# Kernel tuning notes

Measured on AMD Instinct MI355X. Metric: run time of the kernel, lower is better.

## Reference

```python
import math
import jax, jax.numpy as jnp
import numpy as np

B, T, S, H, L, NH = 2, 512, 2048, 768, 32, 12
INTERMED = 4 * H


def _make_pe(max_len, hidden):
    position = np.arange(max_len)[:, None].astype(np.float32)
    div_term = np.exp(np.arange(0, hidden, 2).astype(np.float32) * (-math.log(10000.0) / hidden))
    pe = np.zeros((max_len, hidden), dtype=np.float32)
    pe[:, 0::2] = np.sin(position * div_term)
    pe[:, 1::2] = np.cos(position * div_term)
    return jnp.asarray(pe)


def setup_inputs() -> dict:
    key = jax.random.key(0)
    ks = jax.random.split(key, 10)
    token_reps = jax.random.normal(ks[0], (B, T, H), dtype=jnp.float32)
    starts = jax.random.randint(ks[1], (B, S), 0, T - L)
    lens = jax.random.randint(ks[2], (B, S), 1, L + 1)
    span_ids = jnp.stack([starts, starts + lens], axis=-1)  # (B,S,2)
    span_masks = jax.random.uniform(ks[3], (B, S)) > 0.2
    pe = _make_pe(T, H)
    dummy_query = jax.random.normal(ks[4], (H,), dtype=jnp.float32) * 0.02
    in_proj_w = jax.random.normal(ks[5], (3 * H, H), dtype=jnp.float32) * 0.02
    in_proj_b = jnp.zeros((3 * H,), jnp.float32)
    out_proj_w = jax.random.normal(ks[6], (H, H), dtype=jnp.float32) * 0.02
    out_proj_b = jnp.zeros((H,), jnp.float32)
    norm_g = jnp.ones((H,), jnp.float32)
    norm_b = jnp.zeros((H,), jnp.float32)
    ffn_w1 = jax.random.normal(ks[7], (INTERMED, H), dtype=jnp.float32) * (math.sqrt(2.0 / H))
    ffn_b1 = jnp.zeros((INTERMED,), jnp.float32)
    ffn_w2 = jax.random.normal(ks[8], (H, INTERMED), dtype=jnp.float32) * (math.sqrt(2.0 / INTERMED))
    ffn_b2 = jnp.zeros((H,), jnp.float32)
    return dict(token_reps=token_reps, span_ids=span_ids, span_masks=span_masks,
                pooling=0, pe=pe, dummy_query=dummy_query,
                in_proj_w=in_proj_w, in_proj_b=in_proj_b,
                out_proj_w=out_proj_w, out_proj_b=out_proj_b,
                norm_g=norm_g, norm_b=norm_b,
                ffn_w1=ffn_w1, ffn_b1=ffn_b1, ffn_w2=ffn_w2, ffn_b2=ffn_b2)


def _layernorm(x, g, b, eps=1e-5):
    mu = jnp.mean(x, axis=-1, keepdims=True)
    var = jnp.mean(jnp.square(x - mu), axis=-1, keepdims=True)
    return (x - mu) * jax.lax.rsqrt(var + eps) * g + b


def reference(token_reps, span_ids, span_masks, pooling, pe, dummy_query,
              in_proj_w, in_proj_b, out_proj_w, out_proj_b,
              norm_g, norm_b, ffn_w1, ffn_b1, ffn_w2, ffn_b2):
    b, t, h = token_reps.shape
    s = span_ids.shape[1]
    hd = h // NH
    # positional encoding over the sequence (dropout=0 / eval mode)
    x = token_reps + pe[:t]
    # ragged -> padded gather of span tokens
    starts = span_ids[..., 0]
    lens = (span_ids[..., 1] - starts) * span_masks.astype(span_ids.dtype)  # (B,S)
    ar = jnp.arange(L)
    pos = starts[..., None] + ar                     # (B,S,L)
    valid = ar[None, None, :] < lens[..., None]      # (B,S,L) True = real token
    idx = jnp.clip(pos, 0, t - 1)
    gathered = jax.vmap(lambda xb, ib: xb[ib])(x, idx)   # (B,S,L,H)
    gathered = gathered * valid[..., None]
    # guard fully-masked rows (masked-out / zero-len spans): keep one key valid,
    # output is zeroed at the end anyway (matches torch span_reps[~mask]=0)
    any_v = jnp.any(valid, axis=-1)
    valid = valid.at[..., 0].set(valid[..., 0] | ~any_v)
    # single-query multi-head attention (torch nn.MultiheadAttention math)
    Wq, Wk, Wv = jnp.split(in_proj_w, 3, axis=0)
    bq, bk, bv = jnp.split(in_proj_b, 3, axis=0)
    q = (dummy_query @ Wq.T + bq).reshape(NH, hd)                  # (NH,hd)
    k = (gathered @ Wk.T + bk).reshape(b, s, L, NH, hd)
    v = (gathered @ Wv.T + bv).reshape(b, s, L, NH, hd)
    scores = jnp.einsum('nd,bslnd->bsnl', q, k) / math.sqrt(hd)    # (B,S,NH,L)
    scores = jnp.where(valid[:, :, None, :], scores, -jnp.inf)
    attn = jax.nn.softmax(scores, axis=-1)
    ctx = jnp.einsum('bsnl,bslnd->bsnd', attn, v).reshape(b, s, h)
    attn_out = ctx @ out_proj_w.T + out_proj_b
    # residual + LayerNorm, FFN, residual + same LayerNorm
    x1 = _layernorm(attn_out + dummy_query, norm_g, norm_b)
    ffn = jax.nn.relu(x1 @ ffn_w1.T + ffn_b1) @ ffn_w2.T + ffn_b2
    out = _layernorm(ffn + x1, norm_g, norm_b)
    out = out * span_masks[..., None]
    return out
```

## Files before the change

kernel.cpp:

```cpp
#include <hip/hip_runtime.h>
#include <math.h>

static constexpr int B_  = 2;
static constexpr int T_  = 512;
static constexpr int S_  = 2048;
static constexpr int H_  = 768;
static constexpr int L_  = 32;
static constexpr int NH_ = 12;
static constexpr int HD_ = 64;
static constexpr int IM_ = 3072;

typedef __bf16 bf16x8 __attribute__((ext_vector_type(8)));
typedef float  f32x4  __attribute__((ext_vector_type(4)));

__device__ __forceinline__ float bf2f(unsigned short u) {
    return __uint_as_float(((unsigned)u) << 16);
}
__device__ __forceinline__ unsigned short f2bf(float f) {
    unsigned u = __float_as_uint(f);
    u += 0x7fffu + ((u >> 16) & 1u);
    return (unsigned short)(u >> 16);
}
__device__ __forceinline__ void gl_lds16(const void* g, void* l) {
    __builtin_amdgcn_global_load_lds((const __attribute__((address_space(1))) void*)g,
                                     (__attribute__((address_space(3))) void*)l, 16, 0, 0);
}

__global__ void k_mask(const int* __restrict__ raw, int* __restrict__ mout) {
    __shared__ int bad;
    if (threadIdx.x == 0) bad = 0;
    __syncthreads();
    int v = raw[threadIdx.x];
    if (v != 0 && v != 1) bad = 1;
    __syncthreads();
    int byte_layout = bad;
    const unsigned char* rb = (const unsigned char*)raw;
    for (int i = threadIdx.x; i < B_ * S_; i += 1024)
        mout[i] = byte_layout ? (int)rb[i] : raw[i];
}

__global__ void k_q(const float* __restrict__ dq, const float* __restrict__ w,
                    const float* __restrict__ b, float* __restrict__ q) {
    int wv = threadIdx.x >> 6, lane = threadIdx.x & 63;
    int i = blockIdx.x * 4 + wv;
    const float* row = w + (size_t)i * H_;
    float acc = 0.f;
#pragma unroll
    for (int k = 0; k < 12; ++k) acc += dq[lane + 64 * k] * row[lane + 64 * k];
    for (int m = 32; m; m >>= 1) acc += __shfl_xor(acc, m, 64);
    if (lane == 0) q[i] = acc + b[i];
}

__global__ void k_wqeff(const float* __restrict__ q, const float* __restrict__ w,
                        float* __restrict__ wq) {
    int i = blockIdx.x * 256 + threadIdx.x;
    if (i >= NH_ * H_) return;
    int n = i / H_, hh = i % H_;
    float acc = 0.f;
    for (int d = 0; d < HD_; ++d)
        acc += q[n * HD_ + d] * w[(size_t)(H_ + n * HD_ + d) * H_ + hh];
    wq[i] = acc;
}

__global__ void k_castw(const float* __restrict__ s0, const float* __restrict__ s1,
                        const float* __restrict__ s2, const float* __restrict__ s3,
                        unsigned short* __restrict__ d0, unsigned short* __restrict__ d1,
                        unsigned short* __restrict__ d2, unsigned short* __restrict__ d3) {
    const long n0 = (long)H_ * H_, n2 = (long)IM_ * H_;
    long gid = (long)(blockIdx.x * 256 + threadIdx.x) * 8;
    const float* s; unsigned short* d; long off;
    if (gid < n0)                { s = s0; d = d0; off = gid; }
    else if (gid < 2 * n0)       { s = s1; d = d1; off = gid - n0; }
    else if (gid < 2 * n0 + n2)  { s = s2; d = d2; off = gid - 2 * n0; }
    else                         { s = s3; d = d3; off = gid - 2 * n0 - n2; }
    float4 f0 = *(const float4*)(s + off);
    float4 f1 = *(const float4*)(s + off + 4);
    uint4 o;
    o.x = (unsigned)f2bf(f0.x) | ((unsigned)f2bf(f0.y) << 16);
    o.y = (unsigned)f2bf(f0.z) | ((unsigned)f2bf(f0.w) << 16);
    o.z = (unsigned)f2bf(f1.x) | ((unsigned)f2bf(f1.y) << 16);
    o.w = (unsigned)f2bf(f1.z) | ((unsigned)f2bf(f1.w) << 16);
    *(uint4*)(d + off) = o;
}

__global__ void k_addpe(const float* __restrict__ tr, const float* __restrict__ pe,
                        unsigned short* __restrict__ x) {
    int i = (blockIdx.x * 256 + threadIdx.x) * 8;
    if (i >= B_ * T_ * H_) return;
    float4 a0 = *(const float4*)(tr + i);
    float4 a1 = *(const float4*)(tr + i + 4);
    const float* pp = pe + (i % (T_ * H_));
    float4 p0 = *(const float4*)pp;
    float4 p1 = *(const float4*)(pp + 4);
    uint4 o;
    o.x = (unsigned)f2bf(a0.x + p0.x) | ((unsigned)f2bf(a0.y + p0.y) << 16);
    o.y = (unsigned)f2bf(a0.z + p0.z) | ((unsigned)f2bf(a0.w + p0.w) << 16);
    o.z = (unsigned)f2bf(a1.x + p1.x) | ((unsigned)f2bf(a1.y + p1.y) << 16);
    o.w = (unsigned)f2bf(a1.z + p1.z) | ((unsigned)f2bf(a1.w + p1.w) << 16);
    *(uint4*)(x + i) = o;
}

__global__ void k_stok(const unsigned short* __restrict__ x, const float* __restrict__ wq,
                       float* __restrict__ stok) {
    int bt = blockIdx.x;
    int lane = threadIdx.x & 63, w = threadIdx.x >> 6;
    const unsigned short* xr = x + (size_t)bt * H_;
    float xv[12];
#pragma unroll
    for (int k = 0; k < 12; ++k) xv[k] = bf2f(xr[lane + 64 * k]);
#pragma unroll
    for (int hh = 0; hh < 3; ++hh) {
        int n = w * 3 + hh;
        const float* wr = wq + (size_t)n * H_;
        float acc = 0.f;
#pragma unroll
        for (int k = 0; k < 12; ++k) acc += xv[k] * wr[lane + 64 * k];
        for (int m = 32; m; m >>= 1) acc += __shfl_xor(acc, m, 64);
        if (lane == 0) stok[bt * NH_ + n] = acc;
    }
}

template <bool RELU, bool OBF>
__global__ __launch_bounds__(512)
void gemm_bt(const unsigned short* __restrict__ A, const unsigned short* __restrict__ W,
             const float* __restrict__ bias, void* __restrict__ Cout,
             int M, int N, int K) {
    constexpr int D = 6;
    __shared__ unsigned short As[D * 128 * 32];
    __shared__ unsigned short Bs[D * 128 * 32];
    const int bm = blockIdx.y * 128, bn = blockIdx.x * 128;
    const int tid = threadIdx.x, lane = tid & 63, wid = tid >> 6;
    const int wm = (wid >> 1) * 32, wn = (wid & 1) * 64;
    const int r4 = lane >> 2, kg = (lane & 3) * 8;
    const unsigned short* agp = A + (size_t)(bm + wid * 16 + r4) * K + kg;
    const unsigned short* bgp = W + (size_t)(bn + wid * 16 + r4) * K + kg;

    f32x4 acc[2][4];
#pragma unroll
    for (int i = 0; i < 2; ++i)
#pragma unroll
        for (int j = 0; j < 4; ++j) acc[i][j] = f32x4{0.f, 0.f, 0.f, 0.f};

    const int mrow = lane & 15, kq = (lane >> 4) * 8;
    const int NIT = K >> 5;
    const int npre = NIT < D ? NIT : D;
    for (int p = 0; p < npre; ++p) {
        gl_lds16(agp + (p << 5), As + p * 4096 + wid * 512);
        gl_lds16(bgp + (p << 5), Bs + p * 4096 + wid * 512);
    }
    int buf = 0;
    for (int it = 0; it < NIT; ++it) {
        int rem = NIT - it;
        if (rem >= 6)      asm volatile("s_waitcnt vmcnt(10)" ::: "memory");
        else if (rem == 5) asm volatile("s_waitcnt vmcnt(8)" ::: "memory");
        else if (rem == 4) asm volatile("s_waitcnt vmcnt(6)" ::: "memory");
        else if (rem == 3) asm volatile("s_waitcnt vmcnt(4)" ::: "memory");
        else if (rem == 2) asm volatile("s_waitcnt vmcnt(2)" ::: "memory");
        else               asm volatile("s_waitcnt vmcnt(0)" ::: "memory");
        asm volatile("s_barrier" ::: "memory");
        const unsigned short* cA = As + buf * 4096;
        const unsigned short* cB = Bs + buf * 4096;
        bf16x8 af[2], bfr[4];
#pragma unroll
        for (int i = 0; i < 2; ++i)
            af[i] = *(const bf16x8*)(cA + (wm + i * 16 + mrow) * 32 + kq);
#pragma unroll
        for (int j = 0; j < 4; ++j)
            bfr[j] = *(const bf16x8*)(cB + (wn + j * 16 + mrow) * 32 + kq);
#pragma unroll
        for (int i = 0; i < 2; ++i)
#pragma unroll
            for (int j = 0; j < 4; ++j)
                acc[i][j] = __builtin_amdgcn_mfma_f32_16x16x32_bf16(af[i], bfr[j], acc[i][j], 0, 0, 0);
        asm volatile("s_barrier" ::: "memory");
        if (it + D < NIT) {
            int k0 = (it + D) << 5;
            gl_lds16(agp + k0, As + buf * 4096 + wid * 512);
            gl_lds16(bgp + k0, Bs + buf * 4096 + wid * 512);
        }
        buf = (buf + 1 == D) ? 0 : buf + 1;
    }

    const int lr = (lane >> 4) * 4, lc = lane & 15;
#pragma unroll
    for (int j = 0; j < 4; ++j) {
        int col = bn + wn + j * 16 + lc;
        float bv = bias[col];
#pragma unroll
        for (int i = 0; i < 2; ++i) {
            int row0 = bm + wm + i * 16 + lr;
#pragma unroll
            for (int r = 0; r < 4; ++r) {
                float v = acc[i][j][r] + bv;
                if (RELU) v = fmaxf(v, 0.f);
                if (OBF)
                    ((unsigned short*)Cout)[(size_t)(row0 + r) * N + col] = f2bf(v);
                else
                    ((float*)Cout)[(size_t)(row0 + r) * N + col] = v;
            }
        }
    }
}

__global__ void k_attn(const float* __restrict__ stok, const unsigned short* __restrict__ vtok,
                       const int* __restrict__ span_ids, const int* __restrict__ masks,
                       unsigned short* __restrict__ ctx) {
    int r = blockIdx.x, b = r / S_;
    unsigned short* out = ctx + (size_t)r * H_;
    int tid = threadIdx.x;
    __shared__ float w[NH_][L_];
    __shared__ int idxs[L_];
    __shared__ int s_len;
    if (tid == 0) {
        int m = masks[r];
        int st = span_ids[2 * r], en = span_ids[2 * r + 1];
        int len = m ? (en - st) : 0;
        len = len < 0 ? 0 : (len > L_ ? L_ : len);
        s_len = len;
    }
    __syncthreads();
    int len = s_len;
    if (len == 0) {
        for (int h2 = tid; h2 < H_ / 2; h2 += 256) ((unsigned*)out)[h2] = 0u;
        return;
    }
    if (tid < L_) {
        int p = span_ids[2 * r] + tid;
        idxs[tid] = p < 0 ? 0 : (p > T_ - 1 ? T_ - 1 : p);
    }
    __syncthreads();
    for (int i = tid; i < NH_ * L_; i += 256) {
        int n = i / L_, l = i % L_;
        w[n][l] = (l < len) ? stok[(size_t)(b * T_ + idxs[l]) * NH_ + n] * 0.125f : -INFINITY;
    }
    __syncthreads();
    if (tid < NH_) {
        float mx = -INFINITY;
        for (int l = 0; l < len; ++l) mx = fmaxf(mx, w[tid][l]);
        float sum = 0.f;
        for (int l = 0; l < len; ++l) { float e = __expf(w[tid][l] - mx); w[tid][l] = e; sum += e; }
        float inv = 1.f / sum;
        for (int l = 0; l < len; ++l) w[tid][l] *= inv;
    }
    __syncthreads();
    if (tid < 192) {
        int h0 = tid * 4, n = h0 >> 6;
        float a0 = 0.f, a1 = 0.f, a2 = 0.f, a3 = 0.f;
        for (int l = 0; l < len; ++l) {
            float wl = w[n][l];
            const unsigned short* vr = vtok + (size_t)(b * T_ + idxs[l]) * H_ + h0;
            uint2 u = *(const uint2*)vr;
            a0 += wl * bf2f((unsigned short)(u.x & 0xffff));
            a1 += wl * bf2f((unsigned short)(u.x >> 16));
            a2 += wl * bf2f((unsigned short)(u.y & 0xffff));
            a3 += wl * bf2f((unsigned short)(u.y >> 16));
        }
        uint2 o;
        o.x = (unsigned)f2bf(a0) | ((unsigned)f2bf(a1) << 16);
        o.y = (unsigned)f2bf(a2) | ((unsigned)f2bf(a3) << 16);
        *(uint2*)(out + h0) = o;
    }
}

__global__ void k_ln(const float* __restrict__ inp, const float* __restrict__ res,
                     const float* __restrict__ g, const float* __restrict__ bt,
                     float* __restrict__ outp, unsigned short* __restrict__ outbf,
                     const int* __restrict__ masks, int res_broadcast, int apply_mask) {
    int r = blockIdx.x;
    const float* irow = inp + (size_t)r * H_;
    const float* rrow = res_broadcast ? res : res + (size_t)r * H_;
    float* orow = outp + (size_t)r * H_;
    int tid = threadIdx.x;
    float v[3];
    float lsum = 0.f;
#pragma unroll
    for (int i = 0; i < 3; ++i) {
        int h = tid + 256 * i;
        v[i] = irow[h] + rrow[h];
        lsum += v[i];
    }
    __shared__ float sh[256];
    sh[tid] = lsum;
    __syncthreads();
    for (int st = 128; st > 0; st >>= 1) {
        if (tid < st) sh[tid] += sh[tid + st];
        __syncthreads();
    }
    float mean = sh[0] * (1.f / H_);
    __syncthreads();
    float lvar = 0.f;
#pragma unroll
    for (int i = 0; i < 3; ++i) { float d = v[i] - mean; lvar += d * d; }
    sh[tid] = lvar;
    __syncthreads();
    for (int st = 128; st > 0; st >>= 1) {
        if (tid < st) sh[tid] += sh[tid + st];
        __syncthreads();
    }
    float var = sh[0] * (1.f / H_);
    float scale = rsqrtf(var + 1e-5f);
    float mfac = apply_mask ? (masks[r] ? 1.f : 0.f) : 1.f;
#pragma unroll
    for (int i = 0; i < 3; ++i) {
        int h = tid + 256 * i;
        float o = ((v[i] - mean) * scale * g[h] + bt[h]) * mfac;
        orow[h] = o;
        if (outbf) outbf[(size_t)r * H_ + h] = f2bf(o);
    }
}

extern "C" void kernel_launch(void* const* d_in, const int* in_sizes, int n_in,
                              void* d_out, int out_size, void* d_ws, size_t ws_size,
                              hipStream_t stream) {
    const float* token_reps = (const float*)d_in[0];
    const int*   span_ids   = (const int*)d_in[1];
    const int*   masks_raw  = (const int*)d_in[2];
    const float* pe   = (const float*)d_in[4];
    const float* dq   = (const float*)d_in[5];
    const float* in_w = (const float*)d_in[6];
    const float* in_b = (const float*)d_in[7];
    const float* ow   = (const float*)d_in[8];
    const float* ob   = (const float*)d_in[9];
    const float* g    = (const float*)d_in[10];
    const float* bt   = (const float*)d_in[11];
    const float* w1   = (const float*)d_in[12];
    const float* b1   = (const float*)d_in[13];
    const float* w2   = (const float*)d_in[14];
    const float* b2   = (const float*)d_in[15];

    const int BS = B_ * S_;
    const int BT = B_ * T_;

    float* fws   = (float*)d_ws;
    float* stok  = fws;
    float* qv    = stok + BT * NH_;
    float* wqeff = qv + H_;
    float* A1    = wqeff + NH_ * H_;
    float* x1f   = A1 + (size_t)BS * H_;
    unsigned short* us   = (unsigned short*)(x1f + (size_t)BS * H_);
    unsigned short* xbf  = us;
    unsigned short* vtok = xbf + (size_t)BT * H_;
    unsigned short* ctx  = vtok + (size_t)BT * H_;
    unsigned short* x1bf = ctx + (size_t)BS * H_;
    unsigned short* f1   = x1bf + (size_t)BS * H_;
    unsigned short* wvb  = f1 + (size_t)BS * IM_;
    unsigned short* owb  = wvb + H_ * H_;
    unsigned short* w1b  = owb + H_ * H_;
    unsigned short* w2b  = w1b + IM_ * H_;
    int* maskn = (int*)(w2b + H_ * IM_);
    float* f2 = A1;

    k_mask<<<1, 1024, 0, stream>>>(masks_raw, maskn);
    k_q<<<H_ / 4, 256, 0, stream>>>(dq, in_w, in_b, qv);
    k_wqeff<<<(NH_ * H_ + 255) / 256, 256, 0, stream>>>(qv, in_w, wqeff);
    {
        long total8 = ((long)2 * H_ * H_ + (long)2 * IM_ * H_) / 8;
        k_castw<<<(int)(total8 / 256), 256, 0, stream>>>(
            in_w + (size_t)2 * H_ * H_, ow, w1, w2, wvb, owb, w1b, w2b);
    }
    k_addpe<<<(BT * H_ / 8 + 255) / 256, 256, 0, stream>>>(token_reps, pe, xbf);
    k_stok<<<BT, 256, 0, stream>>>(xbf, wqeff, stok);
    {
        dim3 grid(H_ / 128, BT / 128);
        gemm_bt<false, true><<<grid, 512, 0, stream>>>(xbf, wvb, in_b + 2 * H_, vtok, BT, H_, H_);
    }
    k_attn<<<BS, 256, 0, stream>>>(stok, vtok, span_ids, maskn, ctx);
    {
        dim3 grid(H_ / 128, BS / 128);
        gemm_bt<false, false><<<grid, 512, 0, stream>>>(ctx, owb, ob, A1, BS, H_, H_);
    }
    k_ln<<<BS, 256, 0, stream>>>(A1, dq, g, bt, x1f, x1bf, nullptr, 1, 0);
    {
        dim3 grid(IM_ / 128, BS / 128);
        gemm_bt<true, true><<<grid, 512, 0, stream>>>(x1bf, w1b, b1, f1, BS, IM_, H_);
    }
    {
        dim3 grid(H_ / 128, BS / 128);
        gemm_bt<false, false><<<grid, 512, 0, stream>>>(f1, w2b, b2, f2, BS, H_, IM_);
    }
    k_ln<<<BS, 256, 0, stream>>>(f2, x1f, g, bt, (float*)d_out, nullptr, maskn, 0, 1);
}
```

Baseline: 296.4 us.

## Restructure GEMM to 4 waves with 64x64 warp tiles, K=64 swizzled double buffer

The bf16 GEMM goes from 8 waves with 32x64 warp tiles and a 6-deep K=32 pipeline to 4 waves with 64x64 warp tiles, a K=64 step and 2-stage double buffering. LDS rows are XOR-swizzled to avoid bank conflicts on the wider rows. Each wave now issues more MFMAs per fragment load, giving more register reuse and fewer barriers per unit of K. The price is fewer waves for latency hiding, a shallower prefetch pipeline and higher register pressure from 16 accumulators.

Result: faster. 271.1 us (-8.5%).

```diff
diff --git a/kernel.cpp b/kernel.cpp
--- a/kernel.cpp
+++ b/kernel.cpp
@@ -121,64 +121,79 @@
 }
 
 template <bool RELU, bool OBF>
-__global__ __launch_bounds__(512)
+__global__ __launch_bounds__(256)
 void gemm_bt(const unsigned short* __restrict__ A, const unsigned short* __restrict__ W,
              const float* __restrict__ bias, void* __restrict__ Cout,
              int M, int N, int K) {
-    constexpr int D = 6;
-    __shared__ unsigned short As[D * 128 * 32];
-    __shared__ unsigned short Bs[D * 128 * 32];
+    __shared__ unsigned short As[2 * 8192];
+    __shared__ unsigned short Bs[2 * 8192];
     const int bm = blockIdx.y * 128, bn = blockIdx.x * 128;
     const int tid = threadIdx.x, lane = tid & 63, wid = tid >> 6;
-    const int wm = (wid >> 1) * 32, wn = (wid & 1) * 64;
-    const int r4 = lane >> 2, kg = (lane & 3) * 8;
-    const unsigned short* agp = A + (size_t)(bm + wid * 16 + r4) * K + kg;
-    const unsigned short* bgp = W + (size_t)(bn + wid * 16 + r4) * K + kg;
-
-    f32x4 acc[2][4];
-#pragma unroll
-    for (int i = 0; i < 2; ++i)
+    const int wm = (wid >> 1) * 64, wn = (wid & 1) * 64;
+    const int r8 = lane >> 3, c8 = lane & 7;
+    const int swc = (c8 ^ r8) * 8;
+    const unsigned short* agp = A + (size_t)(bm + wid * 32 + r8) * K + swc;
+    const unsigned short* bgp = W + (size_t)(bn + wid * 32 + r8) * K + swc;
+    unsigned short* lA = As + wid * 2048;
+    unsigned short* lB = Bs + wid * 2048;
+
+    f32x4 acc[4][4];
+#pragma unroll
+    for (int i = 0; i < 4; ++i)
 #pragma unroll
         for (int j = 0; j < 4; ++j) acc[i][j] = f32x4{0.f, 0.f, 0.f, 0.f};
 
-    const int mrow = lane & 15, kq = (lane >> 4) * 8;
-    const int NIT = K >> 5;
-    const int npre = NIT < D ? NIT : D;
-    for (int p = 0; p < npre; ++p) {
-        gl_lds16(agp + (p << 5), As + p * 4096 + wid * 512);
-        gl_lds16(bgp + (p << 5), Bs + p * 4096 + wid * 512);
-    }
-    int buf = 0;
+    const int mrow = lane & 15;
+    const int l7 = lane & 7;
+    const int cq0 = lane >> 4;
+    const int NIT = K >> 6;
+
+#pragma unroll
+    for (int p = 0; p < 2; ++p) {
+        const int k0 = p << 6;
+        const int lo = p * 8192;
+#pragma unroll
+        for (int j = 0; j < 4; ++j) {
+            gl_lds16(agp + (size_t)(8 * j) * K + k0, lA + lo + j * 512);
+            gl_lds16(bgp + (size_t)(8 * j) * K + k0, lB + lo + j * 512);
+        }
+    }
+
     for (int it = 0; it < NIT; ++it) {
-        int rem = NIT - it;
-        if (rem >= 6)      asm volatile("s_waitcnt vmcnt(10)" ::: "memory");
-        else if (rem == 5) asm volatile("s_waitcnt vmcnt(8)" ::: "memory");
-        else if (rem == 4) asm volatile("s_waitcnt vmcnt(6)" ::: "memory");
-        else if (rem == 3) asm volatile("s_waitcnt vmcnt(4)" ::: "memory");
-        else if (rem == 2) asm volatile("s_waitcnt vmcnt(2)" ::: "memory");
-        else               asm volatile("s_waitcnt vmcnt(0)" ::: "memory");
+        if (it < NIT - 1) asm volatile("s_waitcnt vmcnt(8)" ::: "memory");
+        else              asm volatile("s_waitcnt vmcnt(0)" ::: "memory");
         asm volatile("s_barrier" ::: "memory");
-        const unsigned short* cA = As + buf * 4096;
-        const unsigned short* cB = Bs + buf * 4096;
-        bf16x8 af[2], bfr[4];
-#pragma unroll
-        for (int i = 0; i < 2; ++i)
-            af[i] = *(const bf16x8*)(cA + (wm + i * 16 + mrow) * 32 + kq);
-#pragma unroll
-        for (int j = 0; j < 4; ++j)
-            bfr[j] = *(const bf16x8*)(cB + (wn + j * 16 + mrow) * 32 + kq);
-#pragma unroll
-        for (int i = 0; i < 2; ++i)
+        const int lo = (it & 1) * 8192;
+        const unsigned short* cA = As + lo;
+        const unsigned short* cB = Bs + lo;
+        bf16x8 af[2][4], bfr[2][4];
+#pragma unroll
+        for (int s = 0; s < 2; ++s) {
+            const int cq = s * 4 + cq0;
+            const int sw = (cq ^ l7) * 8;
+#pragma unroll
+            for (int i = 0; i < 4; ++i)
+                af[s][i] = *(const bf16x8*)(cA + (wm + i * 16 + mrow) * 64 + sw);
 #pragma unroll
             for (int j = 0; j < 4; ++j)
-                acc[i][j] = __builtin_amdgcn_mfma_f32_16x16x32_bf16(af[i], bfr[j], acc[i][j], 0, 0, 0);
+                bfr[s][j] = *(const bf16x8*)(cB + (wn + j * 16 + mrow) * 64 + sw);
+        }
+#pragma unroll
+        for (int s = 0; s < 2; ++s)
+#pragma unroll
+            for (int i = 0; i < 4; ++i)
+#pragma unroll
+                for (int j = 0; j < 4; ++j)
+                    acc[i][j] = __builtin_amdgcn_mfma_f32_16x16x32_bf16(af[s][i], bfr[s][j], acc[i][j], 0, 0, 0);
         asm volatile("s_barrier" ::: "memory");
-        if (it + D < NIT) {
-            int k0 = (it + D) << 5;
-            gl_lds16(agp + k0, As + buf * 4096 + wid * 512);
-            gl_lds16(bgp + k0, Bs + buf * 4096 + wid * 512);
-        }
-        buf = (buf + 1 == D) ? 0 : buf + 1;
+        if (it + 2 < NIT) {
+            const int k0 = (it + 2) << 6;
+#pragma unroll
+            for (int j = 0; j < 4; ++j) {
+                gl_lds16(agp + (size_t)(8 * j) * K + k0, lA + lo + j * 512);
+                gl_lds16(bgp + (size_t)(8 * j) * K + k0, lB + lo + j * 512);
+            }
+        }
     }
 
     const int lr = (lane >> 4) * 4, lc = lane & 15;
@@ -187,7 +202,7 @@
         int col = bn + wn + j * 16 + lc;
         float bv = bias[col];
 #pragma unroll
-        for (int i = 0; i < 2; ++i) {
+        for (int i = 0; i < 4; ++i) {
             int row0 = bm + wm + i * 16 + lr;
 #pragma unroll
             for (int r = 0; r < 4; ++r) {
@@ -362,21 +377,21 @@
     k_stok<<<BT, 256, 0, stream>>>(xbf, wqeff, stok);
     {
         dim3 grid(H_ / 128, BT / 128);
-        gemm_bt<false, true><<<grid, 512, 0, stream>>>(xbf, wvb, in_b + 2 * H_, vtok, BT, H_, H_);
+        gemm_bt<false, true><<<grid, 256, 0, stream>>>(xbf, wvb, in_b + 2 * H_, vtok, BT, H_, H_);
     }
     k_attn<<<BS, 256, 0, stream>>>(stok, vtok, span_ids, maskn, ctx);
     {
         dim3 grid(H_ / 128, BS / 128);
-        gemm_bt<false, false><<<grid, 512, 0, stream>>>(ctx, owb, ob, A1, BS, H_, H_);
+        gemm_bt<false, false><<<grid, 256, 0, stream>>>(ctx, owb, ob, A1, BS, H_, H_);
     }
     k_ln<<<BS, 256, 0, stream>>>(A1, dq, g, bt, x1f, x1bf, nullptr, 1, 0);
     {
         dim3 grid(IM_ / 128, BS / 128);
-        gemm_bt<true, true><<<grid, 512, 0, stream>>>(x1bf, w1b, b1, f1, BS, IM_, H_);
+        gemm_bt<true, true><<<grid, 256, 0, stream>>>(x1bf, w1b, b1, f1, BS, IM_, H_);
     }
     {
         dim3 grid(H_ / 128, BS / 128);
-        gemm_bt<false, false><<<grid, 512, 0, stream>>>(f1, w2b, b2, f2, BS, H_, IM_);
+        gemm_bt<false, false><<<grid, 256, 0, stream>>>(f1, w2b, b2, f2, BS, H_, IM_);
     }
     k_ln<<<BS, 256, 0, stream>>>(f2, x1f, g, bt, (float*)d_out, nullptr, maskn, 0, 1);
 }
```
